# Performance work log

Hardware: AMD Instinct MI355X
Metric: run time of the kernel (lower is better)

The kernel has to match this reference:

```python
import jax, jax.numpy as jnp
import numpy as np

_INF = -1e30
EPS = 1e-8


def _masked_max(v, mask, axis, keepdims=False):
    return jnp.max(jnp.where(mask == 0, _INF, v), axis=axis, keepdims=keepdims)


def _masked_mean(v, mask, axis, keepdims=False):
    s = jnp.sum(jnp.where(mask == 0, 0.0, v), axis=axis, keepdims=keepdims)
    cnt = jnp.sum(jnp.broadcast_to(mask, v.shape), axis=axis, keepdims=keepdims)
    return s / jnp.clip(cnt, EPS, None)


def _masked_softmax(v, mask):
    return jax.nn.softmax(jnp.where(mask == 0, _INF, v), axis=-1)


def _cos(a, b, axis):
    num = jnp.sum(a * b, axis=axis)
    na = jnp.maximum(jnp.sqrt(jnp.sum(a * a, axis=axis)), EPS)
    nb = jnp.maximum(jnp.sqrt(jnp.sum(b * b, axis=axis)), EPS)
    return num / (na * nb)


def _pairwise_cos(c1, c2):
    # c1:[B,L1,H] c2:[B,L2,H] -> [B,L1,L2]
    dots = jnp.einsum('bih,bjh->bij', c1, c2)
    n1 = jnp.maximum(jnp.linalg.norm(c1, axis=-1), EPS)
    n2 = jnp.maximum(jnp.linalg.norm(c2, axis=-1), EPS)
    return dots / (n1[:, :, None] * n2[:, None, :])


def _mpm(v1, v2, w):
    # v1:[B,L,H], v2:[B,L or 1,H], w:[P,H]
    single = _cos(v1, v2, axis=2)[:, :, None]              # [B,L,1]
    wv1 = w[None, None] * v1[:, :, None, :]                # [B,L,P,H]
    wv2 = w[None, None] * v2[:, :, None, :]                # [B,Lv,P,H]
    multi = _cos(wv1, wv2, axis=3)                         # [B,L,P]
    return single, multi


def _mpm_pairwise(c1, c2, w):
    # w:[P,H] -> cosine [B,L1,L2,P]
    wv1 = w[None, :, None, :] * c1[:, None, :, :]          # [B,P,L1,H]
    wv2 = w[None, :, None, :] * c2[:, None, :, :]          # [B,P,L2,H]
    n1 = jnp.linalg.norm(wv1, axis=3, keepdims=True)       # [B,P,L1,1]
    n2 = jnp.linalg.norm(wv2, axis=3, keepdims=True)       # [B,P,L2,1]
    mul = jnp.einsum('bpih,bpjh->bpij', wv1, wv2)
    denom = jnp.clip(n1 * jnp.swapaxes(n2, 2, 3), EPS, None)
    return jnp.transpose(mul / denom, (0, 2, 3, 1))        # [B,L1,L2,P]


def _bimpm(context_1, mask_1, context_2, mask_2, w_ff, w_fb, w_mp, w_att, w_matt):
    B = context_1.shape[0]
    len1 = jnp.sum(mask_1, axis=1).astype(jnp.int32)
    len2 = jnp.sum(mask_2, axis=1).astype(jnp.int32)
    c1 = context_1 * mask_1[:, :, None]
    c2 = context_2 * mask_2[:, :, None]

    cos_sim = _pairwise_cos(c1, c2)                        # [B,L1,L2]
    m2r = mask_2[:, None, :]
    m1r = mask_1[:, None, :]
    cmax1 = _masked_max(cos_sim, m2r, 2, True)
    cmean1 = _masked_mean(cos_sim, m2r, 2, True)
    cos_t = jnp.swapaxes(cos_sim, 1, 2)
    cmax2 = _masked_max(cos_t, m1r, 2, True)
    cmean2 = _masked_mean(cos_t, m1r, 2, True)

    lp1 = jnp.clip(len1 - 1, 0, None)
    lp2 = jnp.clip(len2 - 1, 0, None)
    c1_fl = c1[jnp.arange(B), lp1][:, None, :]             # [B,1,H]
    c2_fl = c2[jnp.arange(B), lp2][:, None, :]
    c1_bl = c1[:, 0:1, :]
    c2_bl = c2[:, 0:1, :]

    mv1_ff = _mpm(c1, c2_fl, w_ff)
    mv2_ff = _mpm(c2, c1_fl, w_ff)
    mv1_bf = _mpm(c1, c2_bl, w_fb)
    mv2_bf = _mpm(c2, c1_bl, w_fb)

    mm = _mpm_pairwise(c1, c2, w_mp)                       # [B,L1,L2,P]
    mv1_max = _masked_max(mm, mask_2[:, None, :, None], 2)
    mv1_mean = _masked_mean(mm, mask_2[:, None, :, None], 2)
    mm_t = jnp.transpose(mm, (0, 2, 1, 3))
    mv2_max = _masked_max(mm_t, mask_1[:, None, :, None], 2)
    mv2_mean = _masked_mean(mm_t, mask_1[:, None, :, None], 2)

    att_2 = c2[:, None, :, :] * cos_sim[:, :, :, None]     # [B,L1,L2,H]
    att_1 = c1[:, :, None, :] * cos_sim[:, :, :, None]     # [B,L1,L2,H]
    att_mean_2 = _masked_softmax(att_2.sum(axis=2), mask_1[:, :, None])  # [B,L1,H]
    att_mean_1 = _masked_softmax(att_1.sum(axis=1), mask_2[:, :, None])  # [B,L2,H]
    mv1_am = _mpm(c1, att_mean_2, w_att)
    mv2_am = _mpm(c2, att_mean_1, w_att)

    att_max_2 = _masked_max(att_2, mask_2[:, None, :, None], 2)          # [B,L1,H]
    att_max_1 = _masked_max(jnp.transpose(att_1, (0, 2, 1, 3)), mask_1[:, None, :, None], 2)  # [B,L2,H]
    mv1_amx = _mpm(c1, att_max_2, w_matt)
    mv2_amx = _mpm(c2, att_max_1, w_matt)

    mv1 = jnp.concatenate([cmax1, cmean1, *mv1_ff, *mv1_bf, mv1_max, mv1_mean, *mv1_am, *mv1_amx], axis=-1)
    mv2 = jnp.concatenate([cmax2, cmean2, *mv2_ff, *mv2_bf, mv2_max, mv2_mean, *mv2_am, *mv2_amx], axis=-1)
    return jnp.concatenate([mv1, mv2], axis=1)             # [B, L1+L2, 102]


def setup_inputs() -> dict:
    key = jax.random.key(0)
    B, L, H, P = 8, 128, 768, 16
    ks = jax.random.split(key, 8)
    context_1 = jax.random.normal(ks[0], (B, L, H), dtype=jnp.float32)
    context_2 = jax.random.normal(ks[1], (B, L, H), dtype=jnp.float32)
    len1 = jax.random.randint(ks[2], (B,), L // 2, L + 1)
    len2 = jax.random.randint(ks[3], (B,), L // 2, L + 1)
    ar = jnp.arange(L)
    mask_1 = (ar[None, :] < len1[:, None]).astype(jnp.float32)
    mask_2 = (ar[None, :] < len2[:, None]).astype(jnp.float32)
    scale = np.sqrt(2.0 / H).astype(np.float32)
    w_ff = jax.random.normal(ks[4], (P, H), dtype=jnp.float32) * scale
    w_fb = jax.random.normal(ks[5], (P, H), dtype=jnp.float32) * scale
    w_mp = jax.random.normal(ks[6], (P, H), dtype=jnp.float32) * scale
    kk = jax.random.split(ks[7], 2)
    w_att = jax.random.normal(kk[0], (P, H), dtype=jnp.float32) * scale
    w_matt = jax.random.normal(kk[1], (P, H), dtype=jnp.float32) * scale
    return {"context_1": context_1, "mask_1": mask_1, "context_2": context_2, "mask_2": mask_2,
            "w_ff": w_ff, "w_fb": w_fb, "w_mp": w_mp, "w_att": w_att, "w_matt": w_matt}


def reference(context_1, mask_1, context_2, mask_2, w_ff, w_fb, w_mp, w_att, w_matt):
    return _bimpm(context_1, mask_1, context_2, mask_2, w_ff, w_fb, w_mp, w_att, w_matt)
```

## Files before the change

### kernel.cpp

```cpp
#include <hip/hip_runtime.h>

#define Bn 8
#define Ln 128
#define Hn 768
#define Pn 16
#define Dn 102
#define EPSF 1e-8f
#define NINF -1e30f

typedef __attribute__((ext_vector_type(8))) short bfrag8;
typedef __attribute__((ext_vector_type(4))) float f32x4;
union FragU { unsigned u[4]; bfrag8 v; };

#define MFMA16(A,B,C) __builtin_amdgcn_mfma_f32_16x16x32_bf16((A),(B),(C),0,0,0)

__device__ __forceinline__ float wred_sum(float v){
#pragma unroll
  for(int o=32;o>=1;o>>=1) v += __shfl_xor(v,o);
  return v;
}
__device__ __forceinline__ float wred_max(float v){
#pragma unroll
  for(int o=32;o>=1;o>>=1) v = fmaxf(v,__shfl_xor(v,o));
  return v;
}
__device__ __forceinline__ float qred_sum(float v){
  v += __shfl_xor(v,16);
  v += __shfl_xor(v,32);
  return v;
}

__device__ __forceinline__ void split8(const float* x, FragU& H, FragU& L){
  float r[8];
#pragma unroll
  for(int q=0;q<8;q++){
    unsigned hb = __float_as_uint(x[q]) & 0xffff0000u;
    r[q] = x[q] - __uint_as_float(hb);
  }
#pragma unroll
  for(int q=0;q<4;q++){
    H.u[q] = __builtin_amdgcn_perm(__float_as_uint(x[2*q+1]), __float_as_uint(x[2*q]), 0x07060302u);
    L.u[q] = __builtin_amdgcn_perm(__float_as_uint(r[2*q+1]), __float_as_uint(r[2*q]), 0x07060302u);
  }
}

#define GLD_LDS(gp, lp) __builtin_amdgcn_global_load_lds( \
    (const __attribute__((address_space(1))) void*)(gp), \
    (__attribute__((address_space(3))) void*)(lp), 16, 0, 0)

constexpr size_t SZ_MAT   = (size_t)Bn*Ln*Hn;
constexpr size_t OFF_C1F  = 0;
constexpr size_t OFF_C2F  = OFF_C1F + SZ_MAT;
constexpr size_t OFF_COS  = OFF_C2F + SZ_MAT;
constexpr size_t OFF_N1   = OFF_COS + (size_t)Bn*Ln*Ln;
constexpr size_t OFF_N2   = OFF_N1 + (size_t)Bn*Ln;
constexpr size_t OFF_WN   = OFF_N2 + (size_t)Bn*Ln;
constexpr size_t OFF_W2T  = OFF_WN + (size_t)2*5*Bn*Pn*Ln;
constexpr size_t OFF_MVMAX  = OFF_W2T + (size_t)5*Hn*Pn;
constexpr size_t OFF_MVMEAN = OFF_MVMAX + (size_t)2*Bn*Ln*Pn;
constexpr size_t OFF_PART   = OFF_MVMEAN + (size_t)2*Bn*Ln*Pn;
constexpr size_t OFF_LENS   = OFF_PART + (size_t)Bn*Ln*Pn*32*2;
constexpr size_t OFF_C2H    = OFF_LENS + 32;
constexpr size_t OFF_C2L    = OFF_C2H + (size_t)Bn*12*128*64/2;
constexpr size_t OFF_W2F    = OFF_C2L + (size_t)Bn*12*128*64/2;
constexpr size_t OFF_W2B    = OFF_W2F + 12288;

__device__ __forceinline__ size_t wnIdx(int side,int X,int b,int p,int i){
  return ((((size_t)side*5 + X)*Bn + b)*Pn + p)*Ln + i;
}

__global__ __launch_bounds__(256) void k_prep(
    const float* __restrict__ m1, const float* __restrict__ m2,
    const float* __restrict__ wff, const float* __restrict__ wfb,
    const float* __restrict__ wmp, const float* __restrict__ watt,
    const float* __restrict__ wmatt,
    float* __restrict__ W2T, float* __restrict__ W2F, float* __restrict__ W2B,
    int* __restrict__ lens){
  int t = threadIdx.x;
  const float* srcs[5] = {wff,wfb,wmp,watt,wmatt};
  if(blockIdx.x < 8){
    int b = blockIdx.x;
    __shared__ int cnt[2];
    if(t<2) cnt[t]=0;
    __syncthreads();
    if(t<Ln){
      if(m1[b*Ln+t]>0.5f) atomicAdd(&cnt[0],1);
      if(m2[b*Ln+t]>0.5f) atomicAdd(&cnt[1],1);
    }
    __syncthreads();
    if(t==0){
      lens[b]=cnt[0]; lens[8+b]=cnt[1];
      lens[16+b]=max(cnt[0]-1,0); lens[24+b]=max(cnt[1]-1,0);
    }
  } else if(blockIdx.x < 248){
    int idx = (blockIdx.x-8)*256 + t;
    int X = idx/(Pn*Hn);
    int r = idx%(Pn*Hn);
    int h = r/Pn, p = r%Pn;
    float w = srcs[X][p*Hn+h];
    W2T[idx] = w*w;
  } else if(blockIdx.x < 296){
    int idx = (blockIdx.x-248)*256 + t;
    int ksg = idx>>9;
    int r   = idx&511;
    int half= r>>8;
    int li  = (r>>2)&63;
    int e4  = r&3;
    int h = ksg*32 + half*16 + ((li>>4)<<2) + e4;
    int p = li&15;
    float w = wmp[p*Hn+h];
    W2F[idx] = w*w;
  } else {
    int idx = (blockIdx.x-296)*256 + t;
    int X   = idx/12288;
    int r   = idx%12288;
    int hh4 = r>>8;
    int li  = (r>>2)&63;
    int e   = r&3;
    int h = (li>>4)*192 + hh4*4 + e;
    int p = li&15;
    float w = srcs[X][p*Hn+h];
    W2B[idx] = w*w;
  }
}

__global__ __launch_bounds__(256) void k_rows(
    const float* __restrict__ ctx1, const float* __restrict__ m1,
    const float* __restrict__ ctx2, const float* __restrict__ m2,
    const float* __restrict__ W2T,
    float* __restrict__ c1f, float* __restrict__ c2f,
    unsigned short* __restrict__ c2h, unsigned short* __restrict__ c2l,
    float* __restrict__ n1, float* __restrict__ n2, float* __restrict__ wn){
  const int i0 = blockIdx.x*4, b = blockIdx.y, side = blockIdx.z;
  const float* ctx = side? ctx2 : ctx1;
  const float* msk = side? m2 : m1;
  float* dst = side? c2f : c1f;
  float* nD  = side? n2 : n1;
  const int t = threadIdx.x, w = t>>6, l = t&63;

  __shared__ float red4[4][4];
  __shared__ float redX[4][4][16];
  __shared__ float mkS[4];

  if(t<4) mkS[t] = msk[b*Ln+i0+t];

#pragma unroll
  for(int r=0;r<4;r++){
    const int i = i0+r;
    const float mk = msk[b*Ln+i];
    const size_t base = ((size_t)(b*Ln+i))*Hn;
    float ss = 0.f;
#pragma unroll
    for(int k=0;k<3;k++){
      float x = ctx[base + t + 256*k]*mk;
      dst[base + t + 256*k] = x;
      ss = fmaf(x,x,ss);
      if(side==1){
        int h = t+256*k;
        int kc = h>>6, hw = h&63, u = hw>>2, e = hw&3;
        int pos = ((u ^ (i&15))<<2) + e;
        size_t o = ((size_t)(b*12+kc)*128 + i)*64 + pos;
        unsigned hb = __float_as_uint(x) & 0xffff0000u;
        float rem = x - __uint_as_float(hb);
        c2h[o] = (unsigned short)(hb>>16);
        c2l[o] = (unsigned short)(__float_as_uint(rem)>>16);
      }
    }
    ss = wred_sum(ss);
    if(l==0) red4[r][w]=ss;
  }
  __syncthreads();
  if(t<4) nD[b*Ln+i0+t] = sqrtf(fmaxf(red4[t][0]+red4[t][1]+red4[t][2]+red4[t][3],0.f));

  const int pq = t&3, hc = t>>2;
  const int h0 = hc*12;
  float v2r[4][12];
#pragma unroll
  for(int r=0;r<4;r++){
    const float mk = mkS[r];
    const float* src = ctx + ((size_t)(b*Ln+i0+r))*Hn + h0;
#pragma unroll
    for(int q=0;q<3;q++){
      float4 xv = *(const float4*)(src + q*4);
      v2r[r][q*4+0]=xv.x*xv.x*mk; v2r[r][q*4+1]=xv.y*xv.y*mk;
      v2r[r][q*4+2]=xv.z*xv.z*mk; v2r[r][q*4+3]=xv.w*xv.w*mk;
    }
  }
  for(int X=0;X<5;++X){
    float acc[4][4];
#pragma unroll
    for(int r=0;r<4;r++){ acc[r][0]=0.f; acc[r][1]=0.f; acc[r][2]=0.f; acc[r][3]=0.f; }
    const float* wb = W2T + (size_t)X*Hn*Pn + pq*4;
#pragma unroll
    for(int h=0;h<12;h++){
      float4 w4 = *(const float4*)(wb + (size_t)(h0+h)*Pn);
#pragma unroll
      for(int r=0;r<4;r++){
        acc[r][0]=fmaf(w4.x,v2r[r][h],acc[r][0]);
        acc[r][1]=fmaf(w4.y,v2r[r][h],acc[r][1]);
        acc[r][2]=fmaf(w4.z,v2r[r][h],acc[r][2]);
        acc[r][3]=fmaf(w4.w,v2r[r][h],acc[r][3]);
      }
    }
#pragma unroll
    for(int r=0;r<4;r++)
#pragma unroll
      for(int pi=0;pi<4;pi++){
        float v = acc[r][pi];
        v += __shfl_xor(v,4); v += __shfl_xor(v,8);
        v += __shfl_xor(v,16); v += __shfl_xor(v,32);
        acc[r][pi]=v;
      }
    if(l<4){
#pragma unroll
      for(int r=0;r<4;r++)
#pragma unroll
        for(int pi=0;pi<4;pi++) redX[w][l][r*4+pi]=acc[r][pi];
    }
    __syncthreads();
    if(t<64){
      int r = t>>4, p = t&15;
      int pqi = p>>2, pii = p&3;
      float s = redX[0][pqi][r*4+pii]+redX[1][pqi][r*4+pii]
               +redX[2][pqi][r*4+pii]+redX[3][pqi][r*4+pii];
      wn[wnIdx(side,X,b,p,i0+r)] = s;
    }
    __syncthreads();
  }
}

__global__ __launch_bounds__(512) void k_mm(
    const float* __restrict__ c1f,
    const unsigned short* __restrict__ c2h, const unsigned short* __restrict__ c2l,
    const float* __restrict__ W2F, const float* __restrict__ WN,
    const float* __restrict__ n1, const float* __restrict__ n2,
    const float* __restrict__ m1, const float* __restrict__ m2,
    const int* __restrict__ lens,
    float* __restrict__ cosM,
    float* __restrict__ mvmax, float* __restrict__ mvmean,
    float* __restrict__ part){
  const int b = blockIdx.x, ig = blockIdx.y, ibase = ig*4;
  const int t = threadIdx.x, l = t&63;
  const int wid = __builtin_amdgcn_readfirstlane(t>>6);
  const int jtp = wid&3, ihalf = wid>>2;
  const int p = l&15, g4 = l>>4;

  __shared__ __align__(16) unsigned short sB2h[2][128][64];
  __shared__ __align__(16) unsigned short sB2l[2][128][64];
  __shared__ __align__(16) float sw2[2][1024];
  __shared__ __align__(16) float sa[2][4][64];
  __shared__ float sm2s[Ln];
  __shared__ float red0[2][4][2][16][2];

  const size_t c2elem = (size_t)b*12*8192;

  {
#pragma unroll
    for(int k=0;k<2;k++){
      GLD_LDS((const char*)c2h + c2elem*2 + (2*wid+k)*1024 + l*16,
              (char*)&sB2h[0][0][0] + (2*wid+k)*1024);
      GLD_LDS((const char*)c2l + c2elem*2 + (2*wid+k)*1024 + l*16,
              (char*)&sB2l[0][0][0] + (2*wid+k)*1024);
    }
    if(wid>=4){
      int q = wid-4;
      GLD_LDS((const char*)W2F + q*1024 + l*16,
              (char*)&sw2[0][0] + q*1024);
    }
    if(t<Ln) sm2s[t] = m2[b*Ln+t];
    if(t<64){
      int row = t>>4, u = t&15;
      float4 av = *(const float4*)(c1f + ((size_t)(b*Ln+ibase+row))*Hn + u*4);
      *(float4*)&sa[0][row][(u ^ (row&3))<<2] = av;
    }
  }
  __syncthreads();

  f32x4 accE[2][2]; f32x4 accC[2];
#pragma unroll
  for(int q=0;q<2;q++){
    accC[q] = (f32x4){0.f,0.f,0.f,0.f};
#pragma unroll
    for(int ii=0;ii<2;ii++) accE[q][ii] = (f32x4){0.f,0.f,0.f,0.f};
  }

  for(int c=0; c<12; ++c){
    const int cur = c&1, nxt = cur^1;
    const bool more = (c+1<12);
    float4 aN;
    if(more){
      const size_t cb2 = (c2elem + (size_t)(c+1)*8192)*2;
#pragma unroll
      for(int k=0;k<2;k++){
        GLD_LDS((const char*)c2h + cb2 + (2*wid+k)*1024 + l*16,
                (char*)&sB2h[nxt][0][0] + (2*wid+k)*1024);
        GLD_LDS((const char*)c2l + cb2 + (2*wid+k)*1024 + l*16,
                (char*)&sB2l[nxt][0][0] + (2*wid+k)*1024);
      }
      if(wid>=4){
        int q = wid-4;
        GLD_LDS((const char*)W2F + (c+1)*4096 + q*1024 + l*16,
                (char*)&sw2[nxt][0] + q*1024);
      }
      if(t<64){
        int row = t>>4, u = t&15;
        aN = *(const float4*)(c1f + ((size_t)(b*Ln+ibase+row))*Hn + (c+1)*64 + u*4);
      }
    }
#pragma unroll
    for(int ks=0; ks<2; ++ks){
      f32x4 w20 = *(const f32x4*)&sw2[cur][(ks*2+0)*256 + (l<<2)];
      f32x4 w21 = *(const f32x4*)&sw2[cur][(ks*2+1)*256 + (l<<2)];
      FragU Bh[2], Bl[2];
#pragma unroll
      for(int q=0;q<2;q++){
        int jt = jtp + 4*q;
        int j  = jt*16 + p;
        const char* bh = (const char*)&sB2h[cur][0][0] + j*128;
        const char* bl = (const char*)&sB2l[cur][0][0] + j*128;
        int u1 = (ks*8 + g4)     ^ (j&15);
        int u2 = (ks*8 + 4 + g4) ^ (j&15);
        uint2 h0 = *(const uint2*)(bh + (u1<<3));
        uint2 h1 = *(const uint2*)(bh + (u2<<3));
        uint2 l0 = *(const uint2*)(bl + (u1<<3));
        uint2 l1 = *(const uint2*)(bl + (u2<<3));
        Bh[q].u[0]=h0.x; Bh[q].u[1]=h0.y; Bh[q].u[2]=h1.x; Bh[q].u[3]=h1.y;
        Bl[q].u[0]=l0.x; Bl[q].u[1]=l0.y; Bl[q].u[2]=l1.x; Bl[q].u[3]=l1.y;
      }
      if(ihalf==0){
        int ar = p&3;
        const float* sar = &sa[cur][ar][0];
        f32x4 a0 = *(const f32x4*)(sar + (((ks*8+g4)  ^ar)<<2));
        f32x4 a1 = *(const f32x4*)(sar + (((ks*8+4+g4)^ar)<<2));
        float xv[8] = {a0[0],a0[1],a0[2],a0[3], a1[0],a1[1],a1[2],a1[3]};
        FragU Ah, Al; split8(xv, Ah, Al);
#pragma unroll
        for(int q=0;q<2;q++){
          accC[q] = MFMA16(Bh[q].v, Ah.v, accC[q]);
          accC[q] = MFMA16(Bh[q].v, Al.v, accC[q]);
          accC[q] = MFMA16(Bl[q].v, Ah.v, accC[q]);
        }
      }
#pragma unroll
      for(int ii=0;ii<2;ii++){
        int row = ihalf*2+ii;
        const float* sar = &sa[cur][row][0];
        f32x4 a0 = *(const f32x4*)(sar + (((ks*8+g4)  ^(row&3))<<2));
        f32x4 a1 = *(const f32x4*)(sar + (((ks*8+4+g4)^(row&3))<<2));
        float xv[8] = {a0[0]*w20[0], a0[1]*w20[1], a0[2]*w20[2], a0[3]*w20[3],
                       a1[0]*w21[0], a1[1]*w21[1], a1[2]*w21[2], a1[3]*w21[3]};
        FragU Ah, Al; split8(xv, Ah, Al);
#pragma unroll
        for(int q=0;q<2;q++){
          accE[q][ii] = MFMA16(Bh[q].v, Ah.v, accE[q][ii]);
          accE[q][ii] = MFMA16(Bh[q].v, Al.v, accE[q][ii]);
          accE[q][ii] = MFMA16(Bl[q].v, Ah.v, accE[q][ii]);
        }
      }
    }
    if(more && t<64){
      int row = t>>4, u = t&15;
      *(float4*)&sa[nxt][row][(u ^ (row&3))<<2] = aN;
    }
    __syncthreads();
  }

  const int len2 = min(max(lens[8+b],1),Ln);
  float sq1[2][4];
#pragma unroll
  for(int q=0;q<2;q++){
    int jt = jtp+4*q;
#pragma unroll
    for(int r=0;r<4;r++){
      int j = jt*16 + g4*4 + r;
      sq1[q][r] = sqrtf(fmaxf(WN[wnIdx(1,2,b,p,j)],0.f));
    }
  }
  float s1M[2][4], s1S[2][4];
#pragma unroll
  for(int q=0;q<2;q++)
#pragma unroll
    for(int r=0;r<4;r++){ s1M[q][r]=NINF; s1S[q][r]=0.f; }

#pragma unroll
  for(int ii=0;ii<2;ii++){
    int iR = ibase + ihalf*2 + ii;
    float sr = sqrtf(fmaxf(WN[wnIdx(0,2,b,p,iR)],0.f));
    float mr = m1[b*Ln+iR];
    float vmax=NINF, vsum=0.f;
#pragma unroll
    for(int q=0;q<2;q++){
      int jt = jtp+4*q;
#pragma unroll
      for(int r=0;r<4;r++){
        int j = jt*16 + g4*4 + r;
        float ev = accE[q][ii][r] / fmaxf(sr*sq1[q][r], EPSF);
        if(sm2s[j]!=0.f){ vmax=fmaxf(vmax,ev); vsum+=ev; }
        if(mr!=0.f){ s1M[q][r]=fmaxf(s1M[q][r],ev); s1S[q][r]+=ev; }
      }
    }
    vmax = fmaxf(vmax, __shfl_xor(vmax,16)); vmax = fmaxf(vmax, __shfl_xor(vmax,32));
    vsum += __shfl_xor(vsum,16); vsum += __shfl_xor(vsum,32);
    if(l<16){ red0[ihalf][jtp][ii][l][0]=vmax; red0[ihalf][jtp][ii][l][1]=vsum; }
  }
  float* red1 = (float*)&sB2h[0][0][0];
  if(ihalf==1){
#pragma unroll
    for(int q=0;q<2;q++)
#pragma unroll
      for(int r=0;r<4;r++){
        int idx = (((jtp*2+q)*64 + l)*4 + r)*2;
        red1[idx]   = s1M[q][r];
        red1[idx+1] = s1S[q][r];
      }
  }
  __syncthreads();
  if(t<64){
    int ih_=t>>5, ii_=(t>>4)&1, p_=t&15;
    float M=NINF,S=0.f;
#pragma unroll
    for(int jq=0;jq<4;jq++){ M=fmaxf(M,red0[ih_][jq][ii_][p_][0]); S+=red0[ih_][jq][ii_][p_][1]; }
    int iR = ibase + ih_*2 + ii_;
    size_t o = ((size_t)(b*Ln+iR))*Pn + p_;
    mvmax[o]=M; mvmean[o]=S/(float)len2;
  }
  if(ihalf==0){
#pragma unroll
    for(int q=0;q<2;q++){
      int jt = jtp+4*q;
#pragma unroll
      for(int r=0;r<4;r++){
        int j = jt*16 + g4*4 + r;
        int idx = (((jtp*2+q)*64 + l)*4 + r)*2;
        float M = fmaxf(s1M[q][r], red1[idx]);
        float S = s1S[q][r] + red1[idx+1];
        size_t o = ((((size_t)(b*Ln+j))*Pn + p)*32 + ig)*2;
        part[o]=M; part[o+1]=S;
        float nj = fmaxf(n2[b*Ln+j], EPSF);
        if(p<4){
          int iR = ibase + p;
          float ni = fmaxf(n1[b*Ln+iR], EPSF);
          cosM[((size_t)(b*Ln+iR))*Ln + j] = accC[q][r]/(ni*nj);
        }
      }
    }
  }
}

__global__ __launch_bounds__(256) void k_mm2(
    const float* __restrict__ part, const int* __restrict__ lens,
    float* __restrict__ mvmax, float* __restrict__ mvmean){
  int g = blockIdx.x*256 + threadIdx.x;
  int b = g>>11;
  const float4* q = (const float4*)(part + (size_t)g*64);
  float mx = NINF, sm = 0.f;
#pragma unroll
  for(int k=0;k<16;k++){
    float4 v = q[k];
    mx = fmaxf(mx, fmaxf(v.x, v.z));
    sm += v.y + v.w;
  }
  int len1 = min(max(lens[b],1),Ln);
  size_t o = (size_t)Bn*Ln*Pn + g;
  mvmax[o] = mx;
  mvmean[o] = sm/(float)len1;
}

#define HPAD 784
__global__ __launch_bounds__(256) void k_fin(
    const float* __restrict__ c1f, const float* __restrict__ c2f,
    const float* __restrict__ cosM,
    const float* __restrict__ n1, const float* __restrict__ n2,
    const float* __restrict__ wn, const float* __restrict__ W2B,
    const float* __restrict__ mvmax, const float* __restrict__ mvmean,
    const int* __restrict__ lens,
    const float* __restrict__ m1, const float* __restrict__ m2,
    float* __restrict__ out){
  const int x = blockIdx.x, side = x>>3, b = x&7;
  const int r0 = blockIdx.y*2;
  const int t = threadIdx.x, w = t>>6, l = t&63;
  const float* selfF  = side? c2f : c1f;
  const float* otherF = side? c1f : c2f;
  const float* nSelf  = side? n2 : n1;
  const float* nOther = side? n1 : n2;
  const float* mInner = side? m1 : m2;
  const float* mSelfm = side? m2 : m1;
  int lenI = side? lens[b]    : lens[8+b];
  int lpO  = side? lens[16+b] : lens[24+b];
  lenI = min(max(lenI,1),Ln);
  lpO  = min(max(lpO,0),Ln-1);

  __shared__ float cS[2*Ln];
  __shared__ float mS[Ln];
  __shared__ __align__(16) float sV1[2][HPAD];
  __shared__ __align__(16) float sF[HPAD], sB[HPAD];
  __shared__ __align__(16) float sAS[2][HPAD], sAM[2][HPAD];
  __shared__ float red[8][4];

  {
    if(side==0){
      const float* crow = cosM + ((size_t)(b*Ln+r0))*Ln;
      for(int idx=t; idx<2*Ln; idx+=256) cS[idx]=crow[idx];
    } else {
      int jj = t&127, rp = t>>7;
      cS[rp*Ln+jj] = cosM[((size_t)(b*Ln+jj))*Ln + r0+rp];
    }
    if(t<Ln) mS[t]=mInner[b*Ln+t];
    const float4* s4 = (const float4*)(selfF + ((size_t)(b*Ln+r0))*Hn);
    for(int idx=t; idx<2*Hn/4; idx+=256){
      int row = idx/192, q = idx - row*192;
      ((float4*)&sV1[row][0])[q + q/48] = s4[idx];
    }
    const float4* f4 = (const float4*)(otherF + ((size_t)(b*Ln+lpO))*Hn);
    const float4* b4 = (const float4*)(otherF + ((size_t)(b*Ln))*Hn);
    if(t<Hn/4){
      ((float4*)sF)[t + t/48]=f4[t];
      ((float4*)sB)[t + t/48]=b4[t];
    }
  }
  __syncthreads();

  float aS0[3]={0,0,0}, aS1[3]={0,0,0}, aM0[3]={NINF,NINF,NINF}, aM1[3]={NINF,NINF,NINF};
  {
    const float* src = otherF + (size_t)b*Ln*Hn;
#pragma unroll 4
    for(int jj=0; jj<Ln; ++jj){
      float3 vk = ((const float3*)(src + (size_t)jj*Hn))[t];
      float msk = mS[jj];
      float c0=cS[jj], c1v=cS[Ln+jj];
      aS0[0]=fmaf(vk.x,c0 ,aS0[0]); aS0[1]=fmaf(vk.y,c0 ,aS0[1]); aS0[2]=fmaf(vk.z,c0 ,aS0[2]);
      aS1[0]=fmaf(vk.x,c1v,aS1[0]); aS1[1]=fmaf(vk.y,c1v,aS1[1]); aS1[2]=fmaf(vk.z,c1v,aS1[2]);
      if(msk!=0.f){
        aM0[0]=fmaxf(aM0[0],vk.x*c0 ); aM0[1]=fmaxf(aM0[1],vk.y*c0 ); aM0[2]=fmaxf(aM0[2],vk.z*c0 );
        aM1[0]=fmaxf(aM1[0],vk.x*c1v); aM1[1]=fmaxf(aM1[1],vk.y*c1v); aM1[2]=fmaxf(aM1[2],vk.z*c1v);
      }
    }
  }

  {
    float lm0 = fmaxf(fmaxf(aS0[0],aS0[1]),aS0[2]);
    float lm1 = fmaxf(fmaxf(aS1[0],aS1[1]),aS1[2]);
    lm0 = wred_max(lm0); lm1 = wred_max(lm1);
    if(l==0){ red[0][w]=lm0; red[1][w]=lm1; }
  }
  __syncthreads();
  float bm0 = fmaxf(fmaxf(red[0][0],red[0][1]),fmaxf(red[0][2],red[0][3]));
  float bm1 = fmaxf(fmaxf(red[1][0],red[1][1]),fmaxf(red[1][2],red[1][3]));
  __syncthreads();
  float ev0[3], ev1[3];
  {
    float es0=0.f, es1=0.f;
#pragma unroll
    for(int k=0;k<3;k++){
      ev0[k]=expf(aS0[k]-bm0); es0+=ev0[k];
      ev1[k]=expf(aS1[k]-bm1); es1+=ev1[k];
    }
    es0 = wred_sum(es0); es1 = wred_sum(es1);
    if(l==0){ red[0][w]=es0; red[1][w]=es1; }
  }
  __syncthreads();
  {
    float smr0 = mSelfm[b*Ln+r0], smr1 = mSelfm[b*Ln+r0+1];
    float bs0 = red[0][0]+red[0][1]+red[0][2]+red[0][3];
    float bs1 = red[1][0]+red[1][1]+red[1][2]+red[1][3];
    float inv0 = 1.f/fmaxf(bs0,EPSF), inv1 = 1.f/fmaxf(bs1,EPSF);
    const float u = 1.f/(float)Hn;
#pragma unroll
    for(int k=0;k<3;k++){
      int h = 3*t+k;
      int hi = h + ((h/192)<<2);
      sAS[0][hi] = (smr0!=0.f)? ev0[k]*inv0 : u;
      sAS[1][hi] = (smr1!=0.f)? ev1[k]*inv1 : u;
      sAM[0][hi] = aM0[k];
      sAM[1][hi] = aM1[k];
    }
  }
  __syncthreads();

  if(w<2){
    int rr = w;
    float cmx=NINF, csm=0.f;
    float ca = cS[rr*Ln + l], cb = cS[rr*Ln + l + 64];
    if(mS[l]!=0.f){ cmx=ca; csm=ca; }
    if(mS[l+64]!=0.f){ cmx=fmaxf(cmx,cb); csm+=cb; }
    cmx = wred_max(cmx); csm = wred_sum(csm);
    if(l==0){
      float* op = out + ((size_t)((b*2+side)*Ln + r0+rr))*Dn;
      op[0] = cmx;
      op[1] = csm/(float)lenI;
    }
  } else if(w==2){
    int rr = l>>5, qq = l&31, p = qq&15;
    size_t o = ((size_t)((side*Bn+b)*Ln + r0+rr))*Pn + p;
    float* op = out + ((size_t)((b*2+side)*Ln + r0+rr))*Dn;
    if(qq<16) op[36+p] = mvmax[o];
    else      op[52+p] = mvmean[o];
  }

  {
    const int Xids[4] = {0,1,3,4};
    const int offS[4] = {2,19,68,85};
    const int X = Xids[w], offs = offS[w];
    const bool dyn = (w>=2);
    const int p = l&15, hq = l>>4;
    const int hb = hq*196;
    const float4* wB = (const float4*)W2B + (size_t)X*3072 + l;
    float acc0=0.f, acc1=0.f, s00=0.f, s01=0.f;
    float sn0=0.f, sn1=0.f, sna0=0.f, sna1=0.f;
    if(!dyn){
      const float* bvp = (w==0)? sF : sB;
#pragma unroll 4
      for(int h4=0; h4<48; ++h4){
        float4 w4 = wB[h4*64];
        float4 bv = *(const float4*)(bvp + hb + h4*4);
        float4 v0 = *(const float4*)(&sV1[0][hb + h4*4]);
        float4 v1 = *(const float4*)(&sV1[1][hb + h4*4]);
        float pr;
        pr=v0.x*bv.x; acc0=fmaf(w4.x,pr,acc0); s00+=pr;
        pr=v1.x*bv.x; acc1=fmaf(w4.x,pr,acc1); s01+=pr;
        pr=v0.y*bv.y; acc0=fmaf(w4.y,pr,acc0); s00+=pr;
        pr=v1.y*bv.y; acc1=fmaf(w4.y,pr,acc1); s01+=pr;
        pr=v0.z*bv.z; acc0=fmaf(w4.z,pr,acc0); s00+=pr;
        pr=v1.z*bv.z; acc1=fmaf(w4.z,pr,acc1); s01+=pr;
        pr=v0.w*bv.w; acc0=fmaf(w4.w,pr,acc0); s00+=pr;
        pr=v1.w*bv.w; acc1=fmaf(w4.w,pr,acc1); s01+=pr;
      }
    } else {
      const float* bv0p = (w==2)? sAS[0] : sAM[0];
      const float* bv1p = (w==2)? sAS[1] : sAM[1];
#pragma unroll 4
      for(int h4=0; h4<48; ++h4){
        float4 w4 = wB[h4*64];
        float4 b0 = *(const float4*)(bv0p + hb + h4*4);
        float4 b1 = *(const float4*)(bv1p + hb + h4*4);
        float4 v0 = *(const float4*)(&sV1[0][hb + h4*4]);
        float4 v1 = *(const float4*)(&sV1[1][hb + h4*4]);
        float pr0,pr1,bb0,bb1;
        pr0=v0.x*b0.x; pr1=v1.x*b1.x; bb0=b0.x*b0.x; bb1=b1.x*b1.x;
        acc0=fmaf(w4.x,pr0,acc0); acc1=fmaf(w4.x,pr1,acc1);
        sna0=fmaf(w4.x,bb0,sna0); sna1=fmaf(w4.x,bb1,sna1);
        s00+=pr0; s01+=pr1; sn0+=bb0; sn1+=bb1;
        pr0=v0.y*b0.y; pr1=v1.y*b1.y; bb0=b0.y*b0.y; bb1=b1.y*b1.y;
        acc0=fmaf(w4.y,pr0,acc0); acc1=fmaf(w4.y,pr1,acc1);
        sna0=fmaf(w4.y,bb0,sna0); sna1=fmaf(w4.y,bb1,sna1);
        s00+=pr0; s01+=pr1; sn0+=bb0; sn1+=bb1;
        pr0=v0.z*b0.z; pr1=v1.z*b1.z; bb0=b0.z*b0.z; bb1=b1.z*b1.z;
        acc0=fmaf(w4.z,pr0,acc0); acc1=fmaf(w4.z,pr1,acc1);
        sna0=fmaf(w4.z,bb0,sna0); sna1=fmaf(w4.z,bb1,sna1);
        s00+=pr0; s01+=pr1; sn0+=bb0; sn1+=bb1;
        pr0=v0.w*b0.w; pr1=v1.w*b1.w; bb0=b0.w*b0.w; bb1=b1.w*b1.w;
        acc0=fmaf(w4.w,pr0,acc0); acc1=fmaf(w4.w,pr1,acc1);
        sna0=fmaf(w4.w,bb0,sna0); sna1=fmaf(w4.w,bb1,sna1);
        s00+=pr0; s01+=pr1; sn0+=bb0; sn1+=bb1;
      }
    }
    acc0 = qred_sum(acc0); acc1 = qred_sum(acc1);
    s00  = qred_sum(s00);  s01  = qred_sum(s01);
    if(dyn){
      sna0 = qred_sum(sna0); sna1 = qred_sum(sna1);
      sn0  = qred_sum(sn0);  sn1  = qred_sum(sn1);
    }
#pragma unroll
    for(int rr=0; rr<2; ++rr){
      const int r = r0+rr;
      float accv = rr? acc1 : acc0;
      float s0v  = rr? s01  : s00;
      float snav = rr? sna1 : sna0;
      float snv  = rr? sn1  : sn0;
      float* op = out + ((size_t)((b*2+side)*Ln + r))*Dn;
      if(l<16){
        float wa = fmaxf(wn[wnIdx(side,X,b,l,r)],0.f);
        float wb = dyn? fmaxf(snav,0.f)
                      : fmaxf(wn[wnIdx(1-side,X,b,l,(w==0? lpO:0))],0.f);
        float mul = accv/(fmaxf(sqrtf(wa),EPSF)*fmaxf(sqrtf(wb),EPSF));
        op[offs+1+l] = mul;
      }
      if(l==0){
        float nb = dyn? sqrtf(fmaxf(snv,0.f)) : nOther[b*Ln + (w==0? lpO : 0)];
        float nv1 = nSelf[b*Ln+r];
        op[offs] = s0v/(fmaxf(nv1,EPSF)*fmaxf(nb,EPSF));
      }
    }
  }
}

extern "C" void kernel_launch(void* const* d_in, const int* in_sizes, int n_in,
                              void* d_out, int out_size, void* d_ws, size_t ws_size,
                              hipStream_t stream) {
  const float* ctx1 = (const float*)d_in[0];
  const float* m1   = (const float*)d_in[1];
  const float* ctx2 = (const float*)d_in[2];
  const float* m2   = (const float*)d_in[3];
  const float* wff  = (const float*)d_in[4];
  const float* wfb  = (const float*)d_in[5];
  const float* wmp  = (const float*)d_in[6];
  const float* watt = (const float*)d_in[7];
  const float* wmatt= (const float*)d_in[8];
  float* out = (float*)d_out;
  float* W = (float*)d_ws;
  int* lens = (int*)(W + OFF_LENS);
  unsigned short* c2h = (unsigned short*)(W + OFF_C2H);
  unsigned short* c2l = (unsigned short*)(W + OFF_C2L);

  k_prep<<<dim3(8 + 240 + 48 + 240), 256, 0, stream>>>(m1,m2,wff,wfb,wmp,watt,wmatt,
      W+OFF_W2T, W+OFF_W2F, W+OFF_W2B, lens);
  k_rows<<<dim3(Ln/4,Bn,2), 256, 0, stream>>>(ctx1,m1,ctx2,m2, W+OFF_W2T,
      W+OFF_C1F, W+OFF_C2F, c2h, c2l, W+OFF_N1, W+OFF_N2, W+OFF_WN);
  k_mm<<<dim3(Bn, 32), 512, 0, stream>>>(W+OFF_C1F, c2h, c2l,
      W+OFF_W2F, W+OFF_WN, W+OFF_N1, W+OFF_N2, m1, m2, lens,
      W+OFF_COS, W+OFF_MVMAX, W+OFF_MVMEAN, W+OFF_PART);
  k_mm2<<<dim3((Bn*Ln*Pn)/256), 256, 0, stream>>>(W+OFF_PART, lens,
      W+OFF_MVMAX, W+OFF_MVMEAN);
  k_fin<<<dim3(16, Ln/2), 256, 0, stream>>>(W+OFF_C1F, W+OFF_C2F, W+OFF_COS,
      W+OFF_N1, W+OFF_N2, W+OFF_WN, W+OFF_W2B, W+OFF_MVMAX, W+OFF_MVMEAN,
      lens, m1, m2, out);
}
```

Baseline: 170.6 us.

## Process four rows per block in k_fin and bound attention loop by length

Each k_fin block now handles four query rows instead of two, halving the grid. Every streamed row of the other context and every weight float4 is reused across four rows, which cuts global memory traffic. The attentive-sum loop now stops at the valid length instead of iterating all positions under a mask. The cost is more shared memory and registers per block, so occupancy drops and fewer blocks are available to fill the GPU.

```diff
diff --git a/kernel.cpp b/kernel.cpp
--- a/kernel.cpp
+++ b/kernel.cpp
@@ -477,7 +477,7 @@
     const float* __restrict__ m1, const float* __restrict__ m2,
     float* __restrict__ out){
   const int x = blockIdx.x, side = x>>3, b = x&7;
-  const int r0 = blockIdx.y*2;
+  const int r0 = blockIdx.y*4;
   const int t = threadIdx.x, w = t>>6, l = t&63;
   const float* selfF  = side? c2f : c1f;
   const float* otherF = side? c1f : c2f;
@@ -490,24 +490,26 @@
   lenI = min(max(lenI,1),Ln);
   lpO  = min(max(lpO,0),Ln-1);
 
-  __shared__ float cS[2*Ln];
+  __shared__ float cS[4*Ln];
   __shared__ float mS[Ln];
-  __shared__ __align__(16) float sV1[2][HPAD];
+  __shared__ __align__(16) float sV1[4][HPAD];
   __shared__ __align__(16) float sF[HPAD], sB[HPAD];
-  __shared__ __align__(16) float sAS[2][HPAD], sAM[2][HPAD];
-  __shared__ float red[8][4];
+  __shared__ __align__(16) float sAS[4][HPAD], sAM[4][HPAD];
+  __shared__ float redm[4][4], reds[4][4];
 
   {
     if(side==0){
       const float* crow = cosM + ((size_t)(b*Ln+r0))*Ln;
-      for(int idx=t; idx<2*Ln; idx+=256) cS[idx]=crow[idx];
+      for(int idx=t; idx<4*Ln; idx+=256) cS[idx]=crow[idx];
     } else {
-      int jj = t&127, rp = t>>7;
-      cS[rp*Ln+jj] = cosM[((size_t)(b*Ln+jj))*Ln + r0+rp];
+      for(int idx=t; idx<4*Ln; idx+=256){
+        int jj = idx&127, rp = idx>>7;
+        cS[rp*Ln+jj] = cosM[((size_t)(b*Ln+jj))*Ln + r0+rp];
+      }
     }
     if(t<Ln) mS[t]=mInner[b*Ln+t];
     const float4* s4 = (const float4*)(selfF + ((size_t)(b*Ln+r0))*Hn);
-    for(int idx=t; idx<2*Hn/4; idx+=256){
+    for(int idx=t; idx<4*Hn/4; idx+=256){
       int row = idx/192, q = idx - row*192;
       ((float4*)&sV1[row][0])[q + q/48] = s4[idx];
     }
@@ -520,64 +522,72 @@
   }
   __syncthreads();
 
-  float aS0[3]={0,0,0}, aS1[3]={0,0,0}, aM0[3]={NINF,NINF,NINF}, aM1[3]={NINF,NINF,NINF};
+  float aS[4][3], aM[4][3];
+#pragma unroll
+  for(int r=0;r<4;r++)
+#pragma unroll
+    for(int k=0;k<3;k++){ aS[r][k]=0.f; aM[r][k]=NINF; }
   {
     const float* src = otherF + (size_t)b*Ln*Hn;
-#pragma unroll 4
-    for(int jj=0; jj<Ln; ++jj){
+#pragma unroll 2
+    for(int jj=0; jj<lenI; ++jj){
       float3 vk = ((const float3*)(src + (size_t)jj*Hn))[t];
-      float msk = mS[jj];
-      float c0=cS[jj], c1v=cS[Ln+jj];
-      aS0[0]=fmaf(vk.x,c0 ,aS0[0]); aS0[1]=fmaf(vk.y,c0 ,aS0[1]); aS0[2]=fmaf(vk.z,c0 ,aS0[2]);
-      aS1[0]=fmaf(vk.x,c1v,aS1[0]); aS1[1]=fmaf(vk.y,c1v,aS1[1]); aS1[2]=fmaf(vk.z,c1v,aS1[2]);
-      if(msk!=0.f){
-        aM0[0]=fmaxf(aM0[0],vk.x*c0 ); aM0[1]=fmaxf(aM0[1],vk.y*c0 ); aM0[2]=fmaxf(aM0[2],vk.z*c0 );
-        aM1[0]=fmaxf(aM1[0],vk.x*c1v); aM1[1]=fmaxf(aM1[1],vk.y*c1v); aM1[2]=fmaxf(aM1[2],vk.z*c1v);
-      }
+      float c0=cS[jj], c1v=cS[Ln+jj], c2v=cS[2*Ln+jj], c3v=cS[3*Ln+jj];
+      aS[0][0]=fmaf(vk.x,c0 ,aS[0][0]); aS[0][1]=fmaf(vk.y,c0 ,aS[0][1]); aS[0][2]=fmaf(vk.z,c0 ,aS[0][2]);
+      aS[1][0]=fmaf(vk.x,c1v,aS[1][0]); aS[1][1]=fmaf(vk.y,c1v,aS[1][1]); aS[1][2]=fmaf(vk.z,c1v,aS[1][2]);
+      aS[2][0]=fmaf(vk.x,c2v,aS[2][0]); aS[2][1]=fmaf(vk.y,c2v,aS[2][1]); aS[2][2]=fmaf(vk.z,c2v,aS[2][2]);
+      aS[3][0]=fmaf(vk.x,c3v,aS[3][0]); aS[3][1]=fmaf(vk.y,c3v,aS[3][1]); aS[3][2]=fmaf(vk.z,c3v,aS[3][2]);
+      aM[0][0]=fmaxf(aM[0][0],vk.x*c0 ); aM[0][1]=fmaxf(aM[0][1],vk.y*c0 ); aM[0][2]=fmaxf(aM[0][2],vk.z*c0 );
+      aM[1][0]=fmaxf(aM[1][0],vk.x*c1v); aM[1][1]=fmaxf(aM[1][1],vk.y*c1v); aM[1][2]=fmaxf(aM[1][2],vk.z*c1v);
+      aM[2][0]=fmaxf(aM[2][0],vk.x*c2v); aM[2][1]=fmaxf(aM[2][1],vk.y*c2v); aM[2][2]=fmaxf(aM[2][2],vk.z*c2v);
+      aM[3][0]=fmaxf(aM[3][0],vk.x*c3v); aM[3][1]=fmaxf(aM[3][1],vk.y*c3v); aM[3][2]=fmaxf(aM[3][2],vk.z*c3v);
     }
   }
 
   {
-    float lm0 = fmaxf(fmaxf(aS0[0],aS0[1]),aS0[2]);
-    float lm1 = fmaxf(fmaxf(aS1[0],aS1[1]),aS1[2]);
-    lm0 = wred_max(lm0); lm1 = wred_max(lm1);
-    if(l==0){ red[0][w]=lm0; red[1][w]=lm1; }
+#pragma unroll
+    for(int r=0;r<4;r++){
+      float lm = fmaxf(fmaxf(aS[r][0],aS[r][1]),aS[r][2]);
+      lm = wred_max(lm);
+      if(l==0) redm[r][w]=lm;
+    }
   }
   __syncthreads();
-  float bm0 = fmaxf(fmaxf(red[0][0],red[0][1]),fmaxf(red[0][2],red[0][3]));
-  float bm1 = fmaxf(fmaxf(red[1][0],red[1][1]),fmaxf(red[1][2],red[1][3]));
-  __syncthreads();
-  float ev0[3], ev1[3];
+  float bm[4];
+#pragma unroll
+  for(int r=0;r<4;r++)
+    bm[r] = fmaxf(fmaxf(redm[r][0],redm[r][1]),fmaxf(redm[r][2],redm[r][3]));
+  float ev[4][3];
   {
-    float es0=0.f, es1=0.f;
-#pragma unroll
-    for(int k=0;k<3;k++){
-      ev0[k]=expf(aS0[k]-bm0); es0+=ev0[k];
-      ev1[k]=expf(aS1[k]-bm1); es1+=ev1[k];
-    }
-    es0 = wred_sum(es0); es1 = wred_sum(es1);
-    if(l==0){ red[0][w]=es0; red[1][w]=es1; }
+#pragma unroll
+    for(int r=0;r<4;r++){
+      float es=0.f;
+#pragma unroll
+      for(int k=0;k<3;k++){ ev[r][k]=expf(aS[r][k]-bm[r]); es+=ev[r][k]; }
+      es = wred_sum(es);
+      if(l==0) reds[r][w]=es;
+    }
   }
   __syncthreads();
   {
-    float smr0 = mSelfm[b*Ln+r0], smr1 = mSelfm[b*Ln+r0+1];
-    float bs0 = red[0][0]+red[0][1]+red[0][2]+red[0][3];
-    float bs1 = red[1][0]+red[1][1]+red[1][2]+red[1][3];
-    float inv0 = 1.f/fmaxf(bs0,EPSF), inv1 = 1.f/fmaxf(bs1,EPSF);
     const float u = 1.f/(float)Hn;
 #pragma unroll
-    for(int k=0;k<3;k++){
-      int h = 3*t+k;
-      int hi = h + ((h/192)<<2);
-      sAS[0][hi] = (smr0!=0.f)? ev0[k]*inv0 : u;
-      sAS[1][hi] = (smr1!=0.f)? ev1[k]*inv1 : u;
-      sAM[0][hi] = aM0[k];
-      sAM[1][hi] = aM1[k];
+    for(int r=0;r<4;r++){
+      float smr = mSelfm[b*Ln+r0+r];
+      float bs = reds[r][0]+reds[r][1]+reds[r][2]+reds[r][3];
+      float inv = 1.f/fmaxf(bs,EPSF);
+#pragma unroll
+      for(int k=0;k<3;k++){
+        int h = 3*t+k;
+        int hi = h + ((h/192)<<2);
+        sAS[r][hi] = (smr!=0.f)? ev[r][k]*inv : u;
+        sAM[r][hi] = aM[r][k];
+      }
     }
   }
   __syncthreads();
 
-  if(w<2){
+  {
     int rr = w;
     float cmx=NINF, csm=0.f;
     float ca = cS[rr*Ln + l], cb = cS[rr*Ln + l + 64];
@@ -589,8 +599,9 @@
       op[0] = cmx;
       op[1] = csm/(float)lenI;
     }
-  } else if(w==2){
-    int rr = l>>5, qq = l&31, p = qq&15;
+  }
+  if(t<128){
+    int rr = t>>5, qq = t&31, p = qq&15;
     size_t o = ((size_t)((side*Bn+b)*Ln + r0+rr))*Pn + p;
     float* op = out + ((size_t)((b*2+side)*Ln + r0+rr))*Dn;
     if(qq<16) op[36+p] = mvmax[o];
@@ -605,80 +616,65 @@
     const int p = l&15, hq = l>>4;
     const int hb = hq*196;
     const float4* wB = (const float4*)W2B + (size_t)X*3072 + l;
-    float acc0=0.f, acc1=0.f, s00=0.f, s01=0.f;
-    float sn0=0.f, sn1=0.f, sna0=0.f, sna1=0.f;
+    float acc[4]={0,0,0,0}, s0[4]={0,0,0,0};
+    float sna[4]={0,0,0,0}, sn[4]={0,0,0,0};
     if(!dyn){
       const float* bvp = (w==0)? sF : sB;
 #pragma unroll 4
       for(int h4=0; h4<48; ++h4){
         float4 w4 = wB[h4*64];
         float4 bv = *(const float4*)(bvp + hb + h4*4);
-        float4 v0 = *(const float4*)(&sV1[0][hb + h4*4]);
-        float4 v1 = *(const float4*)(&sV1[1][hb + h4*4]);
-        float pr;
-        pr=v0.x*bv.x; acc0=fmaf(w4.x,pr,acc0); s00+=pr;
-        pr=v1.x*bv.x; acc1=fmaf(w4.x,pr,acc1); s01+=pr;
-        pr=v0.y*bv.y; acc0=fmaf(w4.y,pr,acc0); s00+=pr;
-        pr=v1.y*bv.y; acc1=fmaf(w4.y,pr,acc1); s01+=pr;
-        pr=v0.z*bv.z; acc0=fmaf(w4.z,pr,acc0); s00+=pr;
-        pr=v1.z*bv.z; acc1=fmaf(w4.z,pr,acc1); s01+=pr;
-        pr=v0.w*bv.w; acc0=fmaf(w4.w,pr,acc0); s00+=pr;
-        pr=v1.w*bv.w; acc1=fmaf(w4.w,pr,acc1); s01+=pr;
+#pragma unroll
+        for(int r=0;r<4;r++){
+          float4 v = *(const float4*)(&sV1[r][hb + h4*4]);
+          float pr;
+          pr=v.x*bv.x; acc[r]=fmaf(w4.x,pr,acc[r]); s0[r]+=pr;
+          pr=v.y*bv.y; acc[r]=fmaf(w4.y,pr,acc[r]); s0[r]+=pr;
+          pr=v.z*bv.z; acc[r]=fmaf(w4.z,pr,acc[r]); s0[r]+=pr;
+          pr=v.w*bv.w; acc[r]=fmaf(w4.w,pr,acc[r]); s0[r]+=pr;
+        }
       }
     } else {
-      const float* bv0p = (w==2)? sAS[0] : sAM[0];
-      const float* bv1p = (w==2)? sAS[1] : sAM[1];
-#pragma unroll 4
+      const float (*bvp)[HPAD] = (w==2)? sAS : sAM;
+#pragma unroll 2
       for(int h4=0; h4<48; ++h4){
         float4 w4 = wB[h4*64];
-        float4 b0 = *(const float4*)(bv0p + hb + h4*4);
-        float4 b1 = *(const float4*)(bv1p + hb + h4*4);
-        float4 v0 = *(const float4*)(&sV1[0][hb + h4*4]);
-        float4 v1 = *(const float4*)(&sV1[1][hb + h4*4]);
-        float pr0,pr1,bb0,bb1;
-        pr0=v0.x*b0.x; pr1=v1.x*b1.x; bb0=b0.x*b0.x; bb1=b1.x*b1.x;
-        acc0=fmaf(w4.x,pr0,acc0); acc1=fmaf(w4.x,pr1,acc1);
-        sna0=fmaf(w4.x,bb0,sna0); sna1=fmaf(w4.x,bb1,sna1);
-        s00+=pr0; s01+=pr1; sn0+=bb0; sn1+=bb1;
-        pr0=v0.y*b0.y; pr1=v1.y*b1.y; bb0=b0.y*b0.y; bb1=b1.y*b1.y;
-        acc0=fmaf(w4.y,pr0,acc0); acc1=fmaf(w4.y,pr1,acc1);
-        sna0=fmaf(w4.y,bb0,sna0); sna1=fmaf(w4.y,bb1,sna1);
-        s00+=pr0; s01+=pr1; sn0+=bb0; sn1+=bb1;
-        pr0=v0.z*b0.z; pr1=v1.z*b1.z; bb0=b0.z*b0.z; bb1=b1.z*b1.z;
-        acc0=fmaf(w4.z,pr0,acc0); acc1=fmaf(w4.z,pr1,acc1);
-        sna0=fmaf(w4.z,bb0,sna0); sna1=fmaf(w4.z,bb1,sna1);
-        s00+=pr0; s01+=pr1; sn0+=bb0; sn1+=bb1;
-        pr0=v0.w*b0.w; pr1=v1.w*b1.w; bb0=b0.w*b0.w; bb1=b1.w*b1.w;
-        acc0=fmaf(w4.w,pr0,acc0); acc1=fmaf(w4.w,pr1,acc1);
-        sna0=fmaf(w4.w,bb0,sna0); sna1=fmaf(w4.w,bb1,sna1);
-        s00+=pr0; s01+=pr1; sn0+=bb0; sn1+=bb1;
-      }
-    }
-    acc0 = qred_sum(acc0); acc1 = qred_sum(acc1);
-    s00  = qred_sum(s00);  s01  = qred_sum(s01);
-    if(dyn){
-      sna0 = qred_sum(sna0); sna1 = qred_sum(sna1);
-      sn0  = qred_sum(sn0);  sn1  = qred_sum(sn1);
-    }
-#pragma unroll
-    for(int rr=0; rr<2; ++rr){
+#pragma unroll
+        for(int r=0;r<4;r++){
+          float4 bv = *(const float4*)(&bvp[r][hb + h4*4]);
+          float4 v  = *(const float4*)(&sV1[r][hb + h4*4]);
+          float pr, bb;
+          pr=v.x*bv.x; bb=bv.x*bv.x;
+          acc[r]=fmaf(w4.x,pr,acc[r]); sna[r]=fmaf(w4.x,bb,sna[r]); s0[r]+=pr; sn[r]+=bb;
+          pr=v.y*bv.y; bb=bv.y*bv.y;
+          acc[r]=fmaf(w4.y,pr,acc[r]); sna[r]=fmaf(w4.y,bb,sna[r]); s0[r]+=pr; sn[r]+=bb;
+          pr=v.z*bv.z; bb=bv.z*bv.z;
+          acc[r]=fmaf(w4.z,pr,acc[r]); sna[r]=fmaf(w4.z,bb,sna[r]); s0[r]+=pr; sn[r]+=bb;
+          pr=v.w*bv.w; bb=bv.w*bv.w;
+          acc[r]=fmaf(w4.w,pr,acc[r]); sna[r]=fmaf(w4.w,bb,sna[r]); s0[r]+=pr; sn[r]+=bb;
+        }
+      }
+    }
+#pragma unroll
+    for(int r=0;r<4;r++){
+      acc[r]=qred_sum(acc[r]); s0[r]=qred_sum(s0[r]);
+      if(dyn){ sna[r]=qred_sum(sna[r]); sn[r]=qred_sum(sn[r]); }
+    }
+#pragma unroll
+    for(int rr=0; rr<4; ++rr){
       const int r = r0+rr;
-      float accv = rr? acc1 : acc0;
-      float s0v  = rr? s01  : s00;
-      float snav = rr? sna1 : sna0;
-      float snv  = rr? sn1  : sn0;
       float* op = out + ((size_t)((b*2+side)*Ln + r))*Dn;
       if(l<16){
         float wa = fmaxf(wn[wnIdx(side,X,b,l,r)],0.f);
-        float wb = dyn? fmaxf(snav,0.f)
+        float wb = dyn? fmaxf(sna[rr],0.f)
                       : fmaxf(wn[wnIdx(1-side,X,b,l,(w==0? lpO:0))],0.f);
-        float mul = accv/(fmaxf(sqrtf(wa),EPSF)*fmaxf(sqrtf(wb),EPSF));
+        float mul = acc[rr]/(fmaxf(sqrtf(wa),EPSF)*fmaxf(sqrtf(wb),EPSF));
         op[offs+1+l] = mul;
       }
       if(l==0){
-        float nb = dyn? sqrtf(fmaxf(snv,0.f)) : nOther[b*Ln + (w==0? lpO : 0)];
+        float nb = dyn? sqrtf(fmaxf(sn[rr],0.f)) : nOther[b*Ln + (w==0? lpO : 0)];
         float nv1 = nSelf[b*Ln+r];
-        op[offs] = s0v/(fmaxf(nv1,EPSF)*fmaxf(nb,EPSF));
+        op[offs] = s0[rr]/(fmaxf(nv1,EPSF)*fmaxf(nb,EPSF));
       }
     }
   }
@@ -711,7 +707,7 @@
       W+OFF_COS, W+OFF_MVMAX, W+OFF_MVMEAN, W+OFF_PART);
   k_mm2<<<dim3((Bn*Ln*Pn)/256), 256, 0, stream>>>(W+OFF_PART, lens,
       W+OFF_MVMAX, W+OFF_MVMEAN);
-  k_fin<<<dim3(16, Ln/2), 256, 0, stream>>>(W+OFF_C1F, W+OFF_C2F, W+OFF_COS,
+  k_fin<<<dim3(16, Ln/4), 256, 0, stream>>>(W+OFF_C1F, W+OFF_C2F, W+OFF_COS,
       W+OFF_N1, W+OFF_N2, W+OFF_WN, W+OFF_W2B, W+OFF_MVMAX, W+OFF_MVMEAN,
       lens, m1, m2, out);
 }
```

Result: faster. 160.9 us (-5.7%).
